# Kernel tuning notes

Hardware: AMD Instinct MI355X
Metric: run time of the kernel (lower is better)

## Reference

```python
import jax, jax.numpy as jnp
import numpy as np

NUM_HEADS = 8
EMBED = 512
HEAD_DIM = EMBED // NUM_HEADS
B, S = 4, 2048


def setup_inputs() -> dict:
    key = jax.random.key(0)
    ks = jax.random.split(key, 8)
    sc = 0.02
    return {
        "values": jax.random.normal(ks[0], (B, S, EMBED), dtype=jnp.float32),
        "keys": jax.random.normal(ks[1], (B, S, EMBED), dtype=jnp.float32),
        "query": jax.random.normal(ks[2], (B, S, EMBED), dtype=jnp.float32),
        "Wv": jax.random.normal(ks[3], (HEAD_DIM, HEAD_DIM), dtype=jnp.float32) * sc,
        "Wk": jax.random.normal(ks[4], (HEAD_DIM, HEAD_DIM), dtype=jnp.float32) * sc,
        "Wq": jax.random.normal(ks[5], (HEAD_DIM, HEAD_DIM), dtype=jnp.float32) * sc,
        "Wo": jax.random.normal(ks[6], (EMBED, EMBED), dtype=jnp.float32) * sc,
        "bo": jnp.zeros((EMBED,), dtype=jnp.float32),
    }


def reference(values, keys, query, Wv, Wk, Wq, Wo, bo):
    b, s, _ = query.shape
    # split heads: [B, S, H, D]
    v = values.reshape(b, s, NUM_HEADS, HEAD_DIM)
    k = keys.reshape(b, s, NUM_HEADS, HEAD_DIM)
    q = query.reshape(b, s, NUM_HEADS, HEAD_DIM)
    # per-head linear (nn.Linear: x @ W.T), weights shared across heads
    v = jnp.einsum("bshd,ed->bshe", v, Wv)
    k = jnp.einsum("bshd,ed->bshe", k, Wk)
    q = jnp.einsum("bshd,ed->bshe", q, Wq)
    # energy: [B, H, Q, K]
    energy = jnp.einsum("bqhd,bkhd->bhqk", q, k)
    # NOTE: original scales by sqrt(embed_size), not sqrt(head_dim)
    attn = jax.nn.softmax(energy / jnp.sqrt(jnp.float32(EMBED)), axis=-1)
    out = jnp.einsum("bhqk,bkhd->bqhd", attn, v).reshape(b, s, EMBED)
    return out @ Wo.T + bo
```

## Files before the change

### kernel.cpp

```cpp
#include <hip/hip_runtime.h>

#define H 8
#define D 64
#define E 512
#define BATCH 4
#define SEQ 2048

typedef __bf16 bf16v8 __attribute__((ext_vector_type(8)));
typedef float f32v4 __attribute__((ext_vector_type(4)));
typedef unsigned int u32v4 __attribute__((ext_vector_type(4)));
typedef unsigned short u16v4 __attribute__((ext_vector_type(4)));

#define MFMA16(a,b,c) __builtin_amdgcn_mfma_f32_16x16x32_bf16(a,b,c,0,0,0)

#define AS1 __attribute__((address_space(1)))
#define AS3 __attribute__((address_space(3)))
#define GLDS16(g, l) __builtin_amdgcn_global_load_lds((const AS1 void*)(g), (AS3 void*)(l), 16, 0, 0)

static __device__ __forceinline__ unsigned short f2bf(float f) {
  unsigned u = __builtin_bit_cast(unsigned, f);
  u += 0x7fffu + ((u >> 16) & 1u);
  return (unsigned short)(u >> 16);
}

static __device__ __forceinline__ float exp2_hw(float x) {
#if __has_builtin(__builtin_amdgcn_exp2f)
  return __builtin_amdgcn_exp2f(x);
#else
  return exp2f(x);
#endif
}

static __device__ __forceinline__ bf16v8 lds16(const char* p) {
  return __builtin_bit_cast(bf16v8, *(const u32v4*)p);
}

static __device__ __forceinline__ unsigned cvtpk(float a, float b) {
  unsigned r;
  asm("v_cvt_pk_bf16_f32 %0, %1, %2" : "=v"(r) : "v"(a), "v"(b));
  return r;
}

__global__ void prep_all(const float* __restrict__ Wo, const float* __restrict__ Wv,
                         const float* __restrict__ Wq, const float* __restrict__ Wk,
                         const float* __restrict__ v, const float* __restrict__ keys,
                         unsigned short* __restrict__ Wo2, unsigned short* __restrict__ MT,
                         unsigned short* __restrict__ vT, unsigned short* __restrict__ kb) {
  __shared__ float tile[64][65];
  int bx = blockIdx.x;
  int t = threadIdx.x;
  if (bx < 1024) {
    int i = bx * 256 + t;
    int n = i >> 9, c = i & 511;
    int h = c >> 6, d = c & 63;
    float acc = 0.f;
    for (int e = 0; e < 64; ++e) acc += Wo[n*512 + h*64 + e] * Wv[e*64 + d];
    Wo2[n*512 + c] = f2bf(acc);
  } else if (bx < 1040) {
    int i = (bx - 1024) * 256 + t;
    int d2 = i >> 6, d1 = i & 63;
    float acc = 0.f;
    for (int e = 0; e < 64; ++e) acc += Wq[e*64 + d1] * Wk[e*64 + d2];
    MT[d2*64 + d1] = f2bf(acc * 0.06375872536061346f);
  } else {
    int flat = bx - 1040;
    int bh = flat >> 5, sc = flat & 31;
    int b = bh >> 3, h = bh & 7;
    {
      const float* kp = keys + (size_t)flat * 4096;
      unsigned short* ko = kb + (size_t)flat * 4096;
      #pragma unroll
      for (int i = 0; i < 4; ++i) {
        f32v4 x = *(const f32v4*)(kp + (i*256 + t)*4);
        u16v4 o = { f2bf(x[0]), f2bf(x[1]), f2bf(x[2]), f2bf(x[3]) };
        *(u16v4*)(ko + (i*256 + t)*4) = o;
      }
    }
    #pragma unroll
    for (int i = 0; i < 4; ++i) {
      int idx = i*256 + t; int si = idx >> 4, fc = (idx & 15)*4;
      *(f32v4*)&tile[si][fc] =
          *(const f32v4*)(v + (size_t)(b*SEQ + sc*64 + si)*E + h*64 + fc);
    }
    __syncthreads();
    #pragma unroll
    for (int i = 0; i < 4; ++i) {
      int idx = i*256 + t; int d = idx >> 4, s4 = (idx & 15)*4;
      u16v4 o = { f2bf(tile[s4+0][d]), f2bf(tile[s4+1][d]),
                  f2bf(tile[s4+2][d]), f2bf(tile[s4+3][d]) };
      *(u16v4*)(vT + (size_t)(bh*64 + d)*SEQ + sc*64 + s4) = o;
    }
  }
}

__global__ __launch_bounds__(256, 2) void attn(const float* __restrict__ query,
                                               const unsigned short* __restrict__ MT,
                                               const unsigned short* __restrict__ kb,
                                               const unsigned short* __restrict__ vT,
                                               unsigned short* __restrict__ ao) {
  __shared__ __align__(16) char lds[49152];
  int orig = blockIdx.x;
  int workid = (orig & 7) * 64 + (orig >> 3);
  int bh = workid >> 4, qt = workid & 15;
  int b = bh >> 3, h = bh & 7;
  int tid = threadIdx.x, w = tid >> 6, lane = tid & 63, hi = lane >> 4, lo = lane & 15;

  const unsigned short* kbase = kb + (size_t)(b*SEQ)*E + h*64;
  const unsigned short* vbase = vT + (size_t)bh*64*SEQ;
  int srow = tid >> 3, scc = tid & 7;

  #pragma unroll
  for (int i = 0; i < 2; ++i) {
    int row = i*32 + srow;
    int sc = scc ^ (row & 7);
    GLDS16(kbase + (size_t)row*E + sc*8,   lds        + i*4096 + w*1024);
    GLDS16(vbase + (size_t)row*SEQ + sc*8, lds + 8192 + i*4096 + w*1024);
  }
  {
    char* xl = lds + 32768;
    #pragma unroll
    for (int i = 0; i < 8; ++i) {
      int c = i*256 + tid;
      int row = c >> 4, cc = c & 15;
      f32v4 xv = *(const f32v4*)(query + (size_t)(b*SEQ + qt*128 + row)*E + h*64 + cc*4);
      u16v4 o = { f2bf(xv[0]), f2bf(xv[1]), f2bf(xv[2]), f2bf(xv[3]) };
      int off = row*128 + ((((cc >> 1) ^ (row & 7))) << 4) + (cc & 1)*8;
      *(u16v4*)(xl + off) = o;
    }
  }
  __syncthreads();

  bf16v8 qa[2][2];
  {
    const char* xl = lds + 32768;
    bf16v8 qrf[2][2];
    #pragma unroll
    for (int m = 0; m < 2; ++m)
      #pragma unroll
      for (int kk = 0; kk < 2; ++kk) {
        int row = w*32 + m*16 + lo;
        qrf[m][kk] = lds16(xl + row*128 + (((kk*4 + hi) ^ (row & 7)) << 4));
      }
    f32v4 qacc[2][4] = {};
    #pragma unroll
    for (int kk = 0; kk < 2; ++kk)
      #pragma unroll
      for (int nt = 0; nt < 4; ++nt) {
        bf16v8 mtf = *(const bf16v8*)(MT + (nt*16 + lo)*64 + kk*32 + hi*8);
        qacc[0][nt] = MFMA16(mtf, qrf[0][kk], qacc[0][nt]);
        qacc[1][nt] = MFMA16(mtf, qrf[1][kk], qacc[1][nt]);
      }
    #pragma unroll
    for (int m = 0; m < 2; ++m) {
      unsigned qv[2][2][2];
      #pragma unroll
      for (int nt = 0; nt < 4; ++nt) {
        qv[nt >> 1][nt & 1][0] = cvtpk(qacc[m][nt][0], qacc[m][nt][1]);
        qv[nt >> 1][nt & 1][1] = cvtpk(qacc[m][nt][2], qacc[m][nt][3]);
      }
      #pragma unroll
      for (int nt1 = 0; nt1 < 2; ++nt1)
        #pragma unroll
        for (int s = 0; s < 2; ++s) {
          asm("v_permlane32_swap_b32 %0, %1"
              : "+v"(qv[nt1][0][s]), "+v"(qv[nt1][1][s]));
          asm("v_permlane16_swap_b32 %0, %1"
              : "+v"(qv[nt1][0][s]), "+v"(qv[nt1][1][s]));
        }
      #pragma unroll
      for (int kk = 0; kk < 2; ++kk) {
        u32v4 c0 = { qv[kk][0][0], qv[kk][0][1], qv[kk][1][0], qv[kk][1][1] };
        qa[m][kk] = __builtin_bit_cast(bf16v8, c0);
      }
    }
  }

  f32v4 oacc[2][4] = {};
  float lsum[2] = {0.f, 0.f};

  for (int kt = 0; kt < 32; ++kt) {
    const char* klc = lds + (kt & 1)*16384;
    const char* vlc = klc + 8192;
    if (kt < 31) {
      char* kln = lds + ((kt & 1) ^ 1)*16384;
      #pragma unroll
      for (int i = 0; i < 2; ++i) {
        int row = i*32 + srow;
        int sc = scc ^ (row & 7);
        GLDS16(kbase + (size_t)((kt+1)*64 + row)*E + sc*8, kln        + i*4096 + w*1024);
        GLDS16(vbase + (size_t)row*SEQ + (kt+1)*64 + sc*8, kln + 8192 + i*4096 + w*1024);
      }
    }
    f32v4 sacc[2][4] = {};
    __builtin_amdgcn_s_setprio(1);
    #pragma unroll
    for (int nt = 0; nt < 4; ++nt)
      #pragma unroll
      for (int kk = 0; kk < 2; ++kk) {
        int row = nt*16 + lo;
        bf16v8 kf = lds16(klc + row*128 + (((kk*4 + hi) ^ (row & 7)) << 4));
        sacc[0][nt] = MFMA16(kf, qa[0][kk], sacc[0][nt]);
        sacc[1][nt] = MFMA16(kf, qa[1][kk], sacc[1][nt]);
      }
    __builtin_amdgcn_s_setprio(0);
    unsigned wv[2][2][2][2];
    #pragma unroll
    for (int m = 0; m < 2; ++m)
      #pragma unroll
      for (int nt = 0; nt < 4; ++nt) {
        float p0 = exp2_hw(sacc[m][nt][0]);
        float p1 = exp2_hw(sacc[m][nt][1]);
        float p2 = exp2_hw(sacc[m][nt][2]);
        float p3 = exp2_hw(sacc[m][nt][3]);
        lsum[m] += (p0 + p1) + (p2 + p3);
        wv[m][nt >> 1][nt & 1][0] = cvtpk(p0, p1);
        wv[m][nt >> 1][nt & 1][1] = cvtpk(p2, p3);
      }
    #pragma unroll
    for (int m = 0; m < 2; ++m)
      #pragma unroll
      for (int nt1 = 0; nt1 < 2; ++nt1)
        #pragma unroll
        for (int s = 0; s < 2; ++s) {
          asm("v_permlane32_swap_b32 %0, %1"
              : "+v"(wv[m][nt1][0][s]), "+v"(wv[m][nt1][1][s]));
          asm("v_permlane16_swap_b32 %0, %1"
              : "+v"(wv[m][nt1][0][s]), "+v"(wv[m][nt1][1][s]));
        }
    __builtin_amdgcn_s_setprio(1);
    #pragma unroll
    for (int ks = 0; ks < 2; ++ks) {
      u32v4 c0 = { wv[0][ks][0][0], wv[0][ks][0][1], wv[0][ks][1][0], wv[0][ks][1][1] };
      u32v4 c1 = { wv[1][ks][0][0], wv[1][ks][0][1], wv[1][ks][1][0], wv[1][ks][1][1] };
      bf16v8 pb0 = __builtin_bit_cast(bf16v8, c0);
      bf16v8 pb1 = __builtin_bit_cast(bf16v8, c1);
      #pragma unroll
      for (int dt = 0; dt < 4; ++dt) {
        int row = dt*16 + lo;
        bf16v8 vf = lds16(vlc + row*128 + (((ks*4 + hi) ^ (row & 7)) << 4));
        oacc[0][dt] = MFMA16(vf, pb0, oacc[0][dt]);
        oacc[1][dt] = MFMA16(vf, pb1, oacc[1][dt]);
      }
    }
    __builtin_amdgcn_s_setprio(0);
    __syncthreads();
  }
  #pragma unroll
  for (int m = 0; m < 2; ++m) {
    lsum[m] += __shfl_xor(lsum[m], 16);
    lsum[m] += __shfl_xor(lsum[m], 32);
    lsum[m] = __builtin_amdgcn_rcpf(lsum[m]);
  }
  #pragma unroll
  for (int m = 0; m < 2; ++m) {
    int tok = b*SEQ + qt*128 + w*32 + m*16 + lo;
    #pragma unroll
    for (int dt = 0; dt < 4; ++dt) {
      u16v4 o = { f2bf(oacc[m][dt][0] * lsum[m]), f2bf(oacc[m][dt][1] * lsum[m]),
                  f2bf(oacc[m][dt][2] * lsum[m]), f2bf(oacc[m][dt][3] * lsum[m]) };
      *(u16v4*)(ao + (size_t)tok*E + h*64 + dt*16 + 4*hi) = o;
    }
  }
}

__global__ __launch_bounds__(256, 2) void final_gemm(const unsigned short* __restrict__ ao,
                                                     const unsigned short* __restrict__ wo2,
                                                     const float* __restrict__ bo,
                                                     float* __restrict__ out) {
  __shared__ __align__(16) char lds[49152];
  int m0 = blockIdx.x * 64, n0 = blockIdx.y * 128;
  int tid = threadIdx.x, w = tid >> 6, lane = tid & 63, hi = lane >> 4, lo = lane & 15;
  int wm = (w >> 1) * 32, wn = (w & 1) * 64;
  int srow = tid >> 3, scc = tid & 7;
  f32v4 acc[2][4] = {};
  #pragma unroll
  for (int i = 0; i < 2; ++i) {
    int row = i*32 + srow;
    int sc = scc ^ (row & 7);
    GLDS16(ao + (size_t)(m0 + row)*E + sc*8, lds + i*4096 + w*1024);
  }
  #pragma unroll
  for (int i = 0; i < 4; ++i) {
    int row = i*32 + srow;
    int sc = scc ^ (row & 7);
    GLDS16(wo2 + (size_t)(n0 + row)*E + sc*8, lds + 8192 + i*4096 + w*1024);
  }
  __syncthreads();
  for (int kt = 0; kt < 8; ++kt) {
    const char* al = lds + (kt & 1)*24576;
    const char* bl = al + 8192;
    if (kt < 7) {
      char* an = lds + ((kt & 1) ^ 1)*24576;
      #pragma unroll
      for (int i = 0; i < 2; ++i) {
        int row = i*32 + srow;
        int sc = scc ^ (row & 7);
        GLDS16(ao + (size_t)(m0 + row)*E + (kt+1)*64 + sc*8, an + i*4096 + w*1024);
      }
      #pragma unroll
      for (int i = 0; i < 4; ++i) {
        int row = i*32 + srow;
        int sc = scc ^ (row & 7);
        GLDS16(wo2 + (size_t)(n0 + row)*E + (kt+1)*64 + sc*8, an + 8192 + i*4096 + w*1024);
      }
    }
    __builtin_amdgcn_s_setprio(1);
    #pragma unroll
    for (int kk = 0; kk < 2; ++kk) {
      bf16v8 af[2], bfv[4];
      #pragma unroll
      for (int mt = 0; mt < 2; ++mt) {
        int row = wm + mt*16 + lo;
        af[mt] = lds16(al + row*128 + (((kk*4 + hi) ^ (row & 7)) << 4));
      }
      #pragma unroll
      for (int nt = 0; nt < 4; ++nt) {
        int row = wn + nt*16 + lo;
        bfv[nt] = lds16(bl + row*128 + (((kk*4 + hi) ^ (row & 7)) << 4));
      }
      #pragma unroll
      for (int mt = 0; mt < 2; ++mt)
        #pragma unroll
        for (int nt = 0; nt < 4; ++nt)
          acc[mt][nt] = MFMA16(af[mt], bfv[nt], acc[mt][nt]);
    }
    __builtin_amdgcn_s_setprio(0);
    __syncthreads();
  }
  #pragma unroll
  for (int nt = 0; nt < 4; ++nt) {
    float bias = bo[n0 + wn + nt*16 + lo];
    #pragma unroll
    for (int mt = 0; mt < 2; ++mt)
      #pragma unroll
      for (int r = 0; r < 4; ++r)
        out[(size_t)(m0 + wm + mt*16 + 4*hi + r)*E + n0 + wn + nt*16 + lo] =
            acc[mt][nt][r] + bias;
  }
}

extern "C" void kernel_launch(void* const* d_in, const int* in_sizes, int n_in,
                              void* d_out, int out_size, void* d_ws, size_t ws_size,
                              hipStream_t stream) {
  const float* values = (const float*)d_in[0];
  const float* keys   = (const float*)d_in[1];
  const float* query  = (const float*)d_in[2];
  const float* Wv     = (const float*)d_in[3];
  const float* Wk     = (const float*)d_in[4];
  const float* Wq     = (const float*)d_in[5];
  const float* Wo     = (const float*)d_in[6];
  const float* bo     = (const float*)d_in[7];
  float* out = (float*)d_out;
  char* ws = (char*)d_ws;

  unsigned short* MT  = (unsigned short*)(ws);
  unsigned short* Wo2 = (unsigned short*)(ws + 8192);
  unsigned short* kb  = (unsigned short*)(ws + (1u  << 20));
  unsigned short* vT  = (unsigned short*)(ws + (9u  << 20));
  unsigned short* ao  = (unsigned short*)(ws + (17u << 20));

  prep_all  <<<2064, 256, 0, stream>>>(Wo, Wv, Wq, Wk, values, keys, Wo2, MT, vT, kb);
  attn      <<<512,  256, 0, stream>>>(query, MT, kb, vT, ao);
  final_gemm<<<dim3(128, 4), 256, 0, stream>>>(ao, Wo2, bo, out);
}
```

Baseline: 156.2 us.

## Load K/V fragments directly from global memory into registers, dropping LDS staging

Removes the shared-memory double buffer for K and V tiles and the per-iteration block barrier. Each wave now loads its MFMA fragments straight from global memory (through the caches) into registers. The query tile is also loaded and converted to bf16 directly from global memory instead of being staged in LDS. This removes the LDS traffic and synchronisation, but each of the four waves now fetches the same K/V data separately, and nothing prefetches the next tile to hide global-load latency.

```diff
diff --git a/kernel.cpp b/kernel.cpp
--- a/kernel.cpp
+++ b/kernel.cpp
@@ -98,7 +98,6 @@
                                                const unsigned short* __restrict__ kb,
                                                const unsigned short* __restrict__ vT,
                                                unsigned short* __restrict__ ao) {
-  __shared__ __align__(16) char lds[49152];
   int orig = blockIdx.x;
   int workid = (orig & 7) * 64 + (orig >> 3);
   int bh = workid >> 4, qt = workid & 15;
@@ -107,39 +106,21 @@
 
   const unsigned short* kbase = kb + (size_t)(b*SEQ)*E + h*64;
   const unsigned short* vbase = vT + (size_t)bh*64*SEQ;
-  int srow = tid >> 3, scc = tid & 7;
-
-  #pragma unroll
-  for (int i = 0; i < 2; ++i) {
-    int row = i*32 + srow;
-    int sc = scc ^ (row & 7);
-    GLDS16(kbase + (size_t)row*E + sc*8,   lds        + i*4096 + w*1024);
-    GLDS16(vbase + (size_t)row*SEQ + sc*8, lds + 8192 + i*4096 + w*1024);
-  }
-  {
-    char* xl = lds + 32768;
-    #pragma unroll
-    for (int i = 0; i < 8; ++i) {
-      int c = i*256 + tid;
-      int row = c >> 4, cc = c & 15;
-      f32v4 xv = *(const f32v4*)(query + (size_t)(b*SEQ + qt*128 + row)*E + h*64 + cc*4);
-      u16v4 o = { f2bf(xv[0]), f2bf(xv[1]), f2bf(xv[2]), f2bf(xv[3]) };
-      int off = row*128 + ((((cc >> 1) ^ (row & 7))) << 4) + (cc & 1)*8;
-      *(u16v4*)(xl + off) = o;
-    }
-  }
-  __syncthreads();
 
   bf16v8 qa[2][2];
   {
-    const char* xl = lds + 32768;
     bf16v8 qrf[2][2];
     #pragma unroll
     for (int m = 0; m < 2; ++m)
       #pragma unroll
       for (int kk = 0; kk < 2; ++kk) {
-        int row = w*32 + m*16 + lo;
-        qrf[m][kk] = lds16(xl + row*128 + (((kk*4 + hi) ^ (row & 7)) << 4));
+        const float* qp = query + (size_t)(b*SEQ + qt*128 + w*32 + m*16 + lo)*E
+                          + h*64 + kk*32 + hi*8;
+        f32v4 x0 = *(const f32v4*)qp;
+        f32v4 x1 = *(const f32v4*)(qp + 4);
+        u32v4 c = { cvtpk(x0[0], x0[1]), cvtpk(x0[2], x0[3]),
+                    cvtpk(x1[0], x1[1]), cvtpk(x1[2], x1[3]) };
+        qrf[m][kk] = __builtin_bit_cast(bf16v8, c);
       }
     f32v4 qacc[2][4] = {};
     #pragma unroll
@@ -179,28 +160,26 @@
   float lsum[2] = {0.f, 0.f};
 
   for (int kt = 0; kt < 32; ++kt) {
-    const char* klc = lds + (kt & 1)*16384;
-    const char* vlc = klc + 8192;
-    if (kt < 31) {
-      char* kln = lds + ((kt & 1) ^ 1)*16384;
-      #pragma unroll
-      for (int i = 0; i < 2; ++i) {
-        int row = i*32 + srow;
-        int sc = scc ^ (row & 7);
-        GLDS16(kbase + (size_t)((kt+1)*64 + row)*E + sc*8, kln        + i*4096 + w*1024);
-        GLDS16(vbase + (size_t)row*SEQ + (kt+1)*64 + sc*8, kln + 8192 + i*4096 + w*1024);
-      }
-    }
+    bf16v8 kf[4][2];
+    #pragma unroll
+    for (int nt = 0; nt < 4; ++nt)
+      #pragma unroll
+      for (int kk = 0; kk < 2; ++kk)
+        kf[nt][kk] = *(const bf16v8*)(kbase + (size_t)(kt*64 + nt*16 + lo)*E + kk*32 + hi*8);
+    bf16v8 vf[4][2];
+    #pragma unroll
+    for (int dt = 0; dt < 4; ++dt)
+      #pragma unroll
+      for (int ks = 0; ks < 2; ++ks)
+        vf[dt][ks] = *(const bf16v8*)(vbase + (size_t)(dt*16 + lo)*SEQ + kt*64 + ks*32 + hi*8);
     f32v4 sacc[2][4] = {};
     __builtin_amdgcn_s_setprio(1);
     #pragma unroll
     for (int nt = 0; nt < 4; ++nt)
       #pragma unroll
       for (int kk = 0; kk < 2; ++kk) {
-        int row = nt*16 + lo;
-        bf16v8 kf = lds16(klc + row*128 + (((kk*4 + hi) ^ (row & 7)) << 4));
-        sacc[0][nt] = MFMA16(kf, qa[0][kk], sacc[0][nt]);
-        sacc[1][nt] = MFMA16(kf, qa[1][kk], sacc[1][nt]);
+        sacc[0][nt] = MFMA16(kf[nt][kk], qa[0][kk], sacc[0][nt]);
+        sacc[1][nt] = MFMA16(kf[nt][kk], qa[1][kk], sacc[1][nt]);
       }
     __builtin_amdgcn_s_setprio(0);
     unsigned wv[2][2][2][2];
@@ -236,14 +215,11 @@
       bf16v8 pb1 = __builtin_bit_cast(bf16v8, c1);
       #pragma unroll
       for (int dt = 0; dt < 4; ++dt) {
-        int row = dt*16 + lo;
-        bf16v8 vf = lds16(vlc + row*128 + (((ks*4 + hi) ^ (row & 7)) << 4));
-        oacc[0][dt] = MFMA16(vf, pb0, oacc[0][dt]);
-        oacc[1][dt] = MFMA16(vf, pb1, oacc[1][dt]);
+        oacc[0][dt] = MFMA16(vf[dt][ks], pb0, oacc[0][dt]);
+        oacc[1][dt] = MFMA16(vf[dt][ks], pb1, oacc[1][dt]);
       }
     }
     __builtin_amdgcn_s_setprio(0);
-    __syncthreads();
   }
   #pragma unroll
   for (int m = 0; m < 2; ++m) {
```

After: 229.9 us. +47.2%, slower.
